# Optimization experiments

Hardware: AMD Instinct MI355X
Metric: run time of the kernel (lower is better)

## Reference

```python
import jax, jax.numpy as jnp
import numpy as np
import math

DIM = 1536
HEAD_DIM = 128
N_HEADS = DIM // HEAD_DIM
B, S = 2, 2048
F, H, W = 8, 16, 16  # F*H*W == S
MAX_POS = 1024
EPS = 1e-6


def _make_freqs():
    # complex rotary freqs per Wan convention, split [22,21,21] over head_dim/2=64
    c = HEAD_DIM // 2
    sizes = [c - 2 * (c // 3), c // 3, c // 3]
    theta = 10000.0
    parts = []
    for s in sizes:
        inv = 1.0 / theta ** (np.arange(s, dtype=np.float64) / s)
        ang = np.arange(MAX_POS, dtype=np.float64)[:, None] * inv[None, :]
        parts.append(np.stack([np.cos(ang), np.sin(ang)], axis=-1))
    return jnp.asarray(np.concatenate(parts, axis=1), dtype=jnp.float32)  # [MAX_POS, 64, 2]


def setup_inputs() -> dict:
    key = jax.random.key(0)
    ks = jax.random.split(key, 12)
    std = 1.0 / math.sqrt(DIM)
    inp = {
        "x": jax.random.normal(ks[0], (B, S, DIM), jnp.float32),
        "seq_lens": jnp.full((B,), S, jnp.int32),
        "grid_sizes": jnp.tile(jnp.array([[F, H, W]], jnp.int32), (B, 1)),
        "freqs": _make_freqs(),
        "Wq": jax.random.normal(ks[1], (DIM, DIM), jnp.float32) * std,
        "bq": jnp.zeros((DIM,), jnp.float32),
        "Wk": jax.random.normal(ks[2], (DIM, DIM), jnp.float32) * std,
        "bk": jnp.zeros((DIM,), jnp.float32),
        "Wv": jax.random.normal(ks[3], (DIM, DIM), jnp.float32) * std,
        "bv": jnp.zeros((DIM,), jnp.float32),
        "Wo": jax.random.normal(ks[4], (DIM, DIM), jnp.float32) * std,
        "bo": jnp.zeros((DIM,), jnp.float32),
        "wq_norm": jnp.ones((DIM,), jnp.float32),
        "wk_norm": jnp.ones((DIM,), jnp.float32),
    }
    return inp


def _rmsnorm(x, w):
    x32 = x.astype(jnp.float32)
    return x32 * jax.lax.rsqrt(jnp.mean(x32 * x32, axis=-1, keepdims=True) + EPS) * w


def _rope_apply(x, grid_sizes, freqs):
    # x: [B, S, N, D]; grid sizes uniform across batch -> vectorized (no per-sample loop)
    f, h, w = (int(v) for v in np.asarray(grid_sizes)[0])
    s_rot = f * h * w
    Bx, Sx, N, D = x.shape
    c = D // 2
    s0, s1 = c - 2 * (c // 3), c // 3
    cos, sin = freqs[..., 0], freqs[..., 1]

    def grid_cs(t):  # build [s_rot, c] table
        tf = jnp.broadcast_to(t[:f, None, None, :s0], (f, h, w, s0))
        th = jnp.broadcast_to(t[None, :h, None, s0:s0 + s1], (f, h, w, s1))
        tw = jnp.broadcast_to(t[None, None, :w, s0 + s1:s0 + 2 * s1], (f, h, w, s1))
        return jnp.concatenate([tf, th, tw], axis=-1).reshape(s_rot, 1, c)

    fc, fs = grid_cs(cos), grid_cs(sin)  # [s_rot, 1, c]
    xr = x[:, :s_rot].astype(jnp.float32).reshape(Bx, s_rot, N, c, 2)
    a, b = xr[..., 0], xr[..., 1]
    out = jnp.stack([a * fc - b * fs, a * fs + b * fc], axis=-1).reshape(Bx, s_rot, N, D)
    if s_rot < Sx:
        out = jnp.concatenate([out, x[:, s_rot:].astype(jnp.float32)], axis=1)
    return out


def reference(x, seq_lens, grid_sizes, freqs, Wq, bq, Wk, bk, Wv, bv, Wo, bo, wq_norm, wk_norm):
    Bx, Sx, dim = x.shape
    N, D = N_HEADS, HEAD_DIM
    q = _rmsnorm(x @ Wq.T + bq, wq_norm).reshape(Bx, Sx, N, D)
    k = _rmsnorm(x @ Wk.T + bk, wk_norm).reshape(Bx, Sx, N, D)
    v = (x @ Wv.T + bv).reshape(Bx, Sx, N, D)
    q = _rope_apply(q, grid_sizes, freqs)
    k = _rope_apply(k, grid_sizes, freqs)
    scores = jnp.einsum("bsnd,btnd->bnst", q, k) / math.sqrt(D)  # [B,N,S,S]
    kmask = jnp.arange(Sx)[None, :] < seq_lens[:, None]          # [B,S] over keys
    scores = jnp.where(kmask[:, None, None, :], scores, -1e30)
    attn = jax.nn.softmax(scores, axis=-1)
    out = jnp.einsum("bnst,btnd->bsnd", attn, v).reshape(Bx, Sx, dim)
    return out @ Wo.T + bo
```

## Files before the change

kernel.cpp:

```cpp
#include <hip/hip_runtime.h>

typedef __attribute__((ext_vector_type(8))) short bf16x8;
typedef __attribute__((ext_vector_type(8))) unsigned short ushort8;
typedef __attribute__((ext_vector_type(4))) float f32x4;
typedef __attribute__((ext_vector_type(16))) float f32x16;
typedef unsigned short u16;
typedef unsigned int u32;

__device__ inline float bf2f(u16 u) {
    unsigned int x = ((unsigned int)u) << 16;
    float f; __builtin_memcpy(&f, &x, 4); return f;
}
__device__ inline u16 f2bf(float f) {
    unsigned int x; __builtin_memcpy(&x, &f, 4);
    unsigned int r = (x + 0x7FFFu + ((x >> 16) & 1u)) >> 16;
    return (u16)r;
}
__device__ inline u32 cvtpk(float lo, float hi) {
    u32 r;
    asm("v_cvt_pk_bf16_f32 %0, %1, %2" : "=v"(r) : "v"(lo), "v"(hi));
    return r;
}
__device__ inline void store_out(u16* p, float v) { *p = f2bf(v); }
__device__ inline void store_out(float* p, float v) { *p = v; }

__global__ __launch_bounds__(256) void f32_to_bf16_kernel(const float* __restrict__ src,
                                                          u16* __restrict__ dst, int n8) {
    int i = blockIdx.x * 256 + threadIdx.x;
    if (i >= n8) return;
    float4 a = *(const float4*)(src + (size_t)i * 8);
    float4 b = *(const float4*)(src + (size_t)i * 8 + 4);
    ushort8 o;
    o[0] = f2bf(a.x); o[1] = f2bf(a.y); o[2] = f2bf(a.z); o[3] = f2bf(a.w);
    o[4] = f2bf(b.x); o[5] = f2bf(b.y); o[6] = f2bf(b.z); o[7] = f2bf(b.w);
    *(ushort8*)(dst + (size_t)i * 8) = o;
}

__global__ __launch_bounds__(256) void build_rope_kernel(const float* __restrict__ freqs,
                                                         float* __restrict__ rope) {
    int i = blockIdx.x * 256 + threadIdx.x;
    int s = i >> 6, j = i & 63;
    int fi = s >> 8, hi = (s >> 4) & 15, wi = s & 15;
    int pos = (j < 22) ? fi : ((j < 43) ? hi : wi);
    rope[s * 128 + j * 2]     = freqs[pos * 128 + j * 2];
    rope[s * 128 + j * 2 + 1] = freqs[pos * 128 + j * 2 + 1];
}

template <typename OutT>
__global__ __launch_bounds__(256) void gemm_bt(const u16* __restrict__ A, const u16* __restrict__ Bw,
                                               const float* __restrict__ bias, OutT* __restrict__ C,
                                               int M, int N, int K) {
    __shared__ __align__(16) u16 As[128 * 32];
    __shared__ __align__(16) u16 Bs[128 * 32];
    const int tid = threadIdx.x;
    const int w = tid >> 6, l = tid & 63;
    const int lg = l >> 4, li = l & 15;
    const int row0 = blockIdx.x * 128, col0 = blockIdx.y * 128;
    const int wr = (w >> 1) * 64, wc = (w & 1) * 64;

    f32x4 acc[4][4] = {};

    for (int k0 = 0; k0 < K; k0 += 32) {
#pragma unroll
        for (int c = 0; c < 2; ++c) {
            int idx = c * 256 + tid;
            int r = idx >> 2, col8 = (idx & 3) * 8;
            const u16* ga = A + (size_t)(row0 + r) * K + k0 + col8;
            const u16* gb = Bw + (size_t)(col0 + r) * K + k0 + col8;
            __builtin_amdgcn_global_load_lds((const __attribute__((address_space(1))) void*)ga,
                (__attribute__((address_space(3))) void*)((char*)As + c * 4096 + w * 1024), 16, 0, 0);
            __builtin_amdgcn_global_load_lds((const __attribute__((address_space(1))) void*)gb,
                (__attribute__((address_space(3))) void*)((char*)Bs + c * 4096 + w * 1024), 16, 0, 0);
        }
        __syncthreads();
        bf16x8 af[4], bfr[4];
#pragma unroll
        for (int m = 0; m < 4; ++m) af[m] = *(const bf16x8*)(As + (wr + m * 16 + li) * 32 + lg * 8);
#pragma unroll
        for (int n = 0; n < 4; ++n) bfr[n] = *(const bf16x8*)(Bs + (wc + n * 16 + li) * 32 + lg * 8);
#pragma unroll
        for (int m = 0; m < 4; ++m)
#pragma unroll
            for (int n = 0; n < 4; ++n)
                acc[m][n] = __builtin_amdgcn_mfma_f32_16x16x32_bf16(af[m], bfr[n], acc[m][n], 0, 0, 0);
        __syncthreads();
    }

#pragma unroll
    for (int m = 0; m < 4; ++m) {
#pragma unroll
        for (int n = 0; n < 4; ++n) {
#pragma unroll
            for (int j = 0; j < 4; ++j) {
                int r = row0 + wr + m * 16 + lg * 4 + j;
                int cc = col0 + wc + n * 16 + li;
                float v = acc[m][n][j] + bias[cc];
                store_out(&C[(size_t)r * N + cc], v);
            }
        }
    }
}

__global__ __launch_bounds__(256) void rmsrope_kernel(const u16* __restrict__ qkv,
                                                      const float* __restrict__ wq_n,
                                                      const float* __restrict__ wk_n,
                                                      const float* __restrict__ rope,
                                                      u16* __restrict__ qh, u16* __restrict__ kh) {
    int row = blockIdx.x;
    int b = row >> 11, s = row & 2047;
    int t = threadIdx.x;
    const u16* pr = qkv + (size_t)row * 4608;
    int c0 = t * 6;

    float q[6], k[6];
#pragma unroll
    for (int i = 0; i < 3; ++i) {
        ushort2 uq = *(const ushort2*)(pr + c0 + 2 * i);
        ushort2 uk = *(const ushort2*)(pr + 1536 + c0 + 2 * i);
        q[2 * i] = bf2f(uq.x); q[2 * i + 1] = bf2f(uq.y);
        k[2 * i] = bf2f(uk.x); k[2 * i + 1] = bf2f(uk.y);
    }
    float sq = 0.f, sk = 0.f;
#pragma unroll
    for (int i = 0; i < 6; ++i) { sq += q[i] * q[i]; sk += k[i] * k[i]; }
#pragma unroll
    for (int off = 32; off >= 1; off >>= 1) {
        sq += __shfl_down(sq, off);
        sk += __shfl_down(sk, off);
    }
    __shared__ float red[8];
    int w = t >> 6, l = t & 63;
    if (l == 0) { red[w] = sq; red[w + 4] = sk; }
    __syncthreads();
    float rq = rsqrtf((red[0] + red[1] + red[2] + red[3]) * (1.0f / 1536.0f) + 1e-6f);
    float rk = rsqrtf((red[4] + red[5] + red[6] + red[7]) * (1.0f / 1536.0f) + 1e-6f);

#pragma unroll
    for (int i = 0; i < 3; ++i) {
        int c = c0 + 2 * i;
        int h = c >> 7, d = c & 127;
        float cs = rope[s * 128 + d];
        float sn = rope[s * 128 + d + 1];
        float qa = q[2 * i] * rq * wq_n[c], qb = q[2 * i + 1] * rq * wq_n[c + 1];
        float ka = k[2 * i] * rk * wk_n[c], kb = k[2 * i + 1] * rk * wk_n[c + 1];
        size_t o = ((size_t)(b * 12 + h) * 2048 + s) * 128 + d;
        ushort2 qo, ko;
        qo.x = f2bf(qa * cs - qb * sn); qo.y = f2bf(qa * sn + qb * cs);
        ko.x = f2bf(ka * cs - kb * sn); ko.y = f2bf(ka * sn + kb * cs);
        *(ushort2*)(qh + o) = qo;
        *(ushort2*)(kh + o) = ko;
    }
}

__global__ __launch_bounds__(256) void vtrans_kernel(const u16* __restrict__ qkv,
                                                     u16* __restrict__ vt) {
    const int s0 = blockIdx.x * 64;
    const int d0 = blockIdx.y * 64;
    const int bh = blockIdx.z;
    const int b = bh / 12, h = bh % 12;
    const int t = threadIdx.x;

    __shared__ __align__(16) u16 L[64 * 72];

#pragma unroll
    for (int j = 0; j < 2; ++j) {
        int idx = j * 256 + t;
        int s = idx >> 3, c8 = idx & 7;
        ushort8 v8 = *(const ushort8*)(qkv + (size_t)(b * 2048 + s0 + s) * 4608 + 3072 + h * 128 + d0 + c8 * 8);
        int pb = c8 ^ ((s >> 3) & 7);
        *(ushort8*)(L + s * 72 + pb * 8) = v8;
    }
    __syncthreads();
#pragma unroll
    for (int j = 0; j < 2; ++j) {
        int idx = j * 256 + t;
        int d = idx >> 3, s8 = idx & 7;
        ushort8 o;
#pragma unroll
        for (int i = 0; i < 8; ++i) {
            int ps = s8 * 8 + i;
            int v4 = ps & 15;
            int ls = (ps & ~15) | (v4 & 3) | ((v4 & 4) << 1) | ((v4 & 8) >> 1);
            o[i] = L[ls * 72 + ((((d >> 3) ^ (ls >> 3)) & 7) << 3) + (d & 7)];
        }
        *(ushort8*)(vt + (size_t)bh * 128 * 2048 + (size_t)(d0 + d) * 2048 + s0 + s8 * 8) = o;
    }
}

__global__ __launch_bounds__(128, 2) void attn_kernel(const u16* __restrict__ qh, const u16* __restrict__ kh,
                                                      const u16* __restrict__ vt, const int* __restrict__ seq_lens,
                                                      u16* __restrict__ aout) {
    const int qt = blockIdx.x;
    const int bh = blockIdx.y;
    const int b = bh / 12, h = bh % 12;
    const int tid = threadIdx.x;
    const int w = tid >> 6, l = tid & 63;
    const int q5 = l & 31;
    const int hi = l >> 5;
    const int seqlen = seq_lens[b];

    __shared__ __align__(16) char smem[32768];
    u16* Ks = (u16*)smem;
    u16* Vs = (u16*)(smem + 16384);

    const size_t hbase = (size_t)bh * 2048 * 128;
    const u16* kb = kh + hbase;
    const u16* vtb = vt + hbase;

    const int qrow = qt * 64 + w * 32 + q5;
    bf16x8 qf[8];
    {
        const u16* qp = qh + hbase + (size_t)qrow * 128 + hi * 8;
#pragma unroll
        for (int kd = 0; kd < 8; ++kd) qf[kd] = *(const bf16x8*)(qp + kd * 16);
    }

    f32x16 oacc[4] = {};
    float m_run = -3e38f, l_run = 0.f;
    const float c2 = 0.08838834764831845f * 1.44269504088896341f;

    for (int kv0 = 0; kv0 < 2048; kv0 += 64) {
        __syncthreads();
#pragma unroll
        for (int i = 0; i < 8; ++i) {
            int p = i * 128 + tid;
            int kr = p >> 4, kc = p & 15;
            __builtin_amdgcn_global_load_lds(
                (const __attribute__((address_space(1))) void*)(kb + (size_t)(kv0 + kr) * 128 + ((kc ^ (kr & 15)) << 3)),
                (__attribute__((address_space(3))) void*)((char*)Ks + (i * 128 + w * 64) * 16), 16, 0, 0);
            int vr = p >> 3, vc = p & 7;
            __builtin_amdgcn_global_load_lds(
                (const __attribute__((address_space(1))) void*)(vtb + (size_t)vr * 2048 + kv0 + ((vc ^ (vr & 7)) << 3)),
                (__attribute__((address_space(3))) void*)((char*)Vs + (i * 128 + w * 64) * 16), 16, 0, 0);
        }
        __syncthreads();

        f32x16 sacc[2] = {};
#pragma unroll
        for (int t = 0; t < 2; ++t) {
            int row = t * 32 + q5;
#pragma unroll
            for (int kd = 0; kd < 8; ++kd) {
                int bk = (2 * kd + hi) ^ (q5 & 15);
                bf16x8 kf = *(const bf16x8*)(Ks + row * 128 + bk * 8);
                sacc[t] = __builtin_amdgcn_mfma_f32_32x32x16_bf16(kf, qf[kd], sacc[t], 0, 0, 0);
            }
        }

        if (kv0 + 64 > seqlen) {
#pragma unroll
            for (int t = 0; t < 2; ++t)
#pragma unroll
                for (int m = 0; m < 4; ++m)
#pragma unroll
                    for (int r = 0; r < 4; ++r) {
                        int kv = kv0 + t * 32 + m * 8 + hi * 4 + r;
                        if (kv >= seqlen) sacc[t][m * 4 + r] = -1e30f;
                    }
        }

        float pmax = sacc[0][0];
#pragma unroll
        for (int t = 0; t < 2; ++t)
#pragma unroll
            for (int r = 0; r < 16; ++r) pmax = fmaxf(pmax, sacc[t][r]);
        pmax = fmaxf(pmax, __shfl_xor(pmax, 32));

        int defer = __all(pmax <= m_run + 62.7f);
        if (!defer) {
            float mnew = fmaxf(m_run, pmax);
            float alpha = __builtin_amdgcn_exp2f((m_run - mnew) * c2);
#pragma unroll
            for (int dt = 0; dt < 4; ++dt)
#pragma unroll
                for (int r = 0; r < 16; ++r) oacc[dt][r] *= alpha;
            l_run *= alpha;
            m_run = mnew;
        }

        float ls = 0.f;
        u32 Wp[2][4][2];
#pragma unroll
        for (int t = 0; t < 2; ++t)
#pragma unroll
            for (int m = 0; m < 4; ++m) {
                float p0 = __builtin_amdgcn_exp2f((sacc[t][4 * m + 0] - m_run) * c2);
                float p1 = __builtin_amdgcn_exp2f((sacc[t][4 * m + 1] - m_run) * c2);
                float p2 = __builtin_amdgcn_exp2f((sacc[t][4 * m + 2] - m_run) * c2);
                float p3 = __builtin_amdgcn_exp2f((sacc[t][4 * m + 3] - m_run) * c2);
                ls += (p0 + p1) + (p2 + p3);
                Wp[t][m][0] = cvtpk(p0, p1);
                Wp[t][m][1] = cvtpk(p2, p3);
            }
        ls += __shfl_xor(ls, 32);
        l_run += ls;

#pragma unroll
        for (int t = 0; t < 2; ++t)
#pragma unroll
            for (int c = 0; c < 2; ++c) {
                union { u32 u[4]; bf16x8 v; } pu;
                pu.u[0] = Wp[t][2 * c][0]; pu.u[1] = Wp[t][2 * c][1];
                pu.u[2] = Wp[t][2 * c + 1][0]; pu.u[3] = Wp[t][2 * c + 1][1];
                int bk = 4 * t + 2 * c + hi;
#pragma unroll
                for (int dt = 0; dt < 4; ++dt) {
                    int drow = dt * 32 + q5;
                    int pb = bk ^ (drow & 7);
                    bf16x8 vf = *(const bf16x8*)(Vs + drow * 64 + pb * 8);
                    oacc[dt] = __builtin_amdgcn_mfma_f32_32x32x16_bf16(vf, pu.v, oacc[dt], 0, 0, 0);
                }
            }
    }

    __syncthreads();
    u32* Lq = (u32*)smem + w * 2144;
    float inv_l = 1.0f / l_run;
#pragma unroll
    for (int dt = 0; dt < 4; ++dt)
#pragma unroll
        for (int m = 0; m < 4; ++m) {
            u32 w0 = cvtpk(oacc[dt][4 * m + 0] * inv_l, oacc[dt][4 * m + 1] * inv_l);
            u32 w1 = cvtpk(oacc[dt][4 * m + 2] * inv_l, oacc[dt][4 * m + 3] * inv_l);
            int widx = dt * 16 + 4 * m + 2 * hi;
            Lq[q5 * 67 + widx] = w0;
            Lq[q5 * 67 + widx + 1] = w1;
        }
    __builtin_amdgcn_s_waitcnt(0);
#pragma unroll
    for (int pp = 0; pp < 8; ++pp) {
        int qq = pp * 4 + (l >> 4);
        int cc = l & 15;
        union { u32 u[4]; ushort8 v; } ou;
        ou.u[0] = Lq[qq * 67 + cc * 4 + 0];
        ou.u[1] = Lq[qq * 67 + cc * 4 + 1];
        ou.u[2] = Lq[qq * 67 + cc * 4 + 2];
        ou.u[3] = Lq[qq * 67 + cc * 4 + 3];
        size_t off = ((size_t)(b * 2048 + qt * 64 + w * 32 + qq)) * 1536 + h * 128 + cc * 8;
        *(ushort8*)(aout + off) = ou.v;
    }
}

extern "C" void kernel_launch(void* const* d_in, const int* in_sizes, int n_in,
                              void* d_out, int out_size, void* d_ws, size_t ws_size,
                              hipStream_t stream) {
    const float* x    = (const float*)d_in[0];
    const int* seqlen = (const int*)d_in[1];
    const float* freqs = (const float*)d_in[3];
    const float* Wq = (const float*)d_in[4];  const float* bq = (const float*)d_in[5];
    const float* Wk = (const float*)d_in[6];  const float* bk = (const float*)d_in[7];
    const float* Wv = (const float*)d_in[8];  const float* bv = (const float*)d_in[9];
    const float* Wo = (const float*)d_in[10]; const float* bo = (const float*)d_in[11];
    const float* wqn = (const float*)d_in[12];
    const float* wkn = (const float*)d_in[13];
    float* out = (float*)d_out;

    char* ws = (char*)d_ws;
    u16*   xb   = (u16*)(ws);
    u16*   wqkv = (u16*)(ws + 12582912);
    u16*   wob  = (u16*)(ws + 26738688);
    float* bqkv = (float*)(ws + 31457280);
    float* rope = (float*)(ws + 31475712);
    u16*   qkv  = (u16*)(ws + 32524288);
    u16*   qhb  = (u16*)(ws + 70273024);
    u16*   khb  = (u16*)(ws + 82855936);
    u16*   vtb  = (u16*)(ws + 95438848);
    u16*   aob  = (u16*)(ws + 108021760);

    f32_to_bf16_kernel<<<3072, 256, 0, stream>>>(x, xb, 786432);
    f32_to_bf16_kernel<<<1152, 256, 0, stream>>>(Wq, wqkv, 294912);
    f32_to_bf16_kernel<<<1152, 256, 0, stream>>>(Wk, wqkv + 2359296, 294912);
    f32_to_bf16_kernel<<<1152, 256, 0, stream>>>(Wv, wqkv + 4718592, 294912);
    f32_to_bf16_kernel<<<1152, 256, 0, stream>>>(Wo, wob, 294912);
    hipMemcpyAsync(bqkv,        bq, 1536 * 4, hipMemcpyDeviceToDevice, stream);
    hipMemcpyAsync(bqkv + 1536, bk, 1536 * 4, hipMemcpyDeviceToDevice, stream);
    hipMemcpyAsync(bqkv + 3072, bv, 1536 * 4, hipMemcpyDeviceToDevice, stream);
    build_rope_kernel<<<512, 256, 0, stream>>>(freqs, rope);

    gemm_bt<u16><<<dim3(32, 36), 256, 0, stream>>>(xb, wqkv, bqkv, qkv, 4096, 4608, 1536);
    rmsrope_kernel<<<4096, 256, 0, stream>>>(qkv, wqn, wkn, rope, qhb, khb);
    vtrans_kernel<<<dim3(32, 2, 24), 256, 0, stream>>>(qkv, vtb);
    attn_kernel<<<dim3(32, 24), 128, 0, stream>>>(qhb, khb, vtb, seqlen, aob);
    gemm_bt<float><<<dim3(32, 12), 256, 0, stream>>>(aob, wob, bo, out, 4096, 1536, 1536);
}
```

Measured before the change: 249.4 us.

## Pipeline GEMM and attention LDS loads, widen attention blocks, fuse weight conversions

The GEMM now uses a triple-buffered LDS ring, issuing global-to-LDS loads two tiles ahead with vmcnt waits and raw barriers instead of full syncthreads. The attention kernel moves to 4 waves per block covering 128 queries, with double-buffered K/V tiles and setprio around the MFMA sections, so memory latency overlaps compute and each K/V tile is shared by more queries. The four weight-conversion launches are merged into one kernel. In exchange, LDS use grows (48KB GEMM, 64KB attention), which may cap occupancy, and there are half as many attention blocks (384).

```diff
diff --git a/kernel.cpp b/kernel.cpp
--- a/kernel.cpp
+++ b/kernel.cpp
@@ -36,6 +36,21 @@
     *(ushort8*)(dst + (size_t)i * 8) = o;
 }
 
+__global__ __launch_bounds__(256) void wconv_kernel(const float* __restrict__ Wq, const float* __restrict__ Wk,
+                                                    const float* __restrict__ Wv, const float* __restrict__ Wo,
+                                                    u16* __restrict__ wqkv, u16* __restrict__ wob) {
+    int i = blockIdx.x * 256 + threadIdx.x;
+    int seg = i / 294912, j = i - seg * 294912;
+    const float* src = (seg == 0) ? Wq : (seg == 1) ? Wk : (seg == 2) ? Wv : Wo;
+    u16* dst = (seg < 3) ? (wqkv + (size_t)seg * 2359296) : wob;
+    float4 a = *(const float4*)(src + (size_t)j * 8);
+    float4 b = *(const float4*)(src + (size_t)j * 8 + 4);
+    ushort8 o;
+    o[0] = f2bf(a.x); o[1] = f2bf(a.y); o[2] = f2bf(a.z); o[3] = f2bf(a.w);
+    o[4] = f2bf(b.x); o[5] = f2bf(b.y); o[6] = f2bf(b.z); o[7] = f2bf(b.w);
+    *(ushort8*)(dst + (size_t)j * 8) = o;
+}
+
 __global__ __launch_bounds__(256) void build_rope_kernel(const float* __restrict__ freqs,
                                                          float* __restrict__ rope) {
     int i = blockIdx.x * 256 + threadIdx.x;
@@ -50,40 +65,63 @@
 __global__ __launch_bounds__(256) void gemm_bt(const u16* __restrict__ A, const u16* __restrict__ Bw,
                                                const float* __restrict__ bias, OutT* __restrict__ C,
                                                int M, int N, int K) {
-    __shared__ __align__(16) u16 As[128 * 32];
-    __shared__ __align__(16) u16 Bs[128 * 32];
+    __shared__ __align__(16) u16 As[3][4096];
+    __shared__ __align__(16) u16 Bs[3][4096];
     const int tid = threadIdx.x;
     const int w = tid >> 6, l = tid & 63;
     const int lg = l >> 4, li = l & 15;
     const int row0 = blockIdx.x * 128, col0 = blockIdx.y * 128;
     const int wr = (w >> 1) * 64, wc = (w & 1) * 64;
+    const int nt = K >> 5;
 
     f32x4 acc[4][4] = {};
 
-    for (int k0 = 0; k0 < K; k0 += 32) {
+    auto STAGE = [&](int bi, int t) {
+        int k0 = t << 5;
 #pragma unroll
         for (int c = 0; c < 2; ++c) {
             int idx = c * 256 + tid;
             int r = idx >> 2, col8 = (idx & 3) * 8;
-            const u16* ga = A + (size_t)(row0 + r) * K + k0 + col8;
-            const u16* gb = Bw + (size_t)(col0 + r) * K + k0 + col8;
-            __builtin_amdgcn_global_load_lds((const __attribute__((address_space(1))) void*)ga,
-                (__attribute__((address_space(3))) void*)((char*)As + c * 4096 + w * 1024), 16, 0, 0);
-            __builtin_amdgcn_global_load_lds((const __attribute__((address_space(1))) void*)gb,
-                (__attribute__((address_space(3))) void*)((char*)Bs + c * 4096 + w * 1024), 16, 0, 0);
-        }
-        __syncthreads();
-        bf16x8 af[4], bfr[4];
-#pragma unroll
-        for (int m = 0; m < 4; ++m) af[m] = *(const bf16x8*)(As + (wr + m * 16 + li) * 32 + lg * 8);
-#pragma unroll
-        for (int n = 0; n < 4; ++n) bfr[n] = *(const bf16x8*)(Bs + (wc + n * 16 + li) * 32 + lg * 8);
-#pragma unroll
-        for (int m = 0; m < 4; ++m)
-#pragma unroll
-            for (int n = 0; n < 4; ++n)
-                acc[m][n] = __builtin_amdgcn_mfma_f32_16x16x32_bf16(af[m], bfr[n], acc[m][n], 0, 0, 0);
-        __syncthreads();
+            __builtin_amdgcn_global_load_lds(
+                (const __attribute__((address_space(1))) void*)(A + (size_t)(row0 + r) * K + k0 + col8),
+                (__attribute__((address_space(3))) void*)((char*)&As[0][0] + bi * 8192 + c * 4096 + w * 1024), 16, 0, 0);
+            __builtin_amdgcn_global_load_lds(
+                (const __attribute__((address_space(1))) void*)(Bw + (size_t)(col0 + r) * K + k0 + col8),
+                (__attribute__((address_space(3))) void*)((char*)&Bs[0][0] + bi * 8192 + c * 4096 + w * 1024), 16, 0, 0);
+        }
+    };
+
+    STAGE(0, 0);
+    STAGE(1, 1);
+    for (int tb = 0; tb < nt; tb += 3) {
+#pragma unroll
+        for (int j = 0; j < 3; ++j) {
+            const int t = tb + j;
+            if (t + 2 < nt) {
+                STAGE((j + 2) % 3, t + 2);
+                asm volatile("s_waitcnt vmcnt(8)" ::: "memory");
+            } else if (t + 1 < nt) {
+                asm volatile("s_waitcnt vmcnt(4)" ::: "memory");
+            } else {
+                asm volatile("s_waitcnt vmcnt(0)" ::: "memory");
+            }
+            __builtin_amdgcn_s_barrier();
+            __builtin_amdgcn_sched_barrier(0);
+            const u16* as = &As[j][0];
+            const u16* bs = &Bs[j][0];
+            bf16x8 af[4], bfr[4];
+#pragma unroll
+            for (int m = 0; m < 4; ++m) af[m] = *(const bf16x8*)(as + (wr + m * 16 + li) * 32 + lg * 8);
+#pragma unroll
+            for (int n = 0; n < 4; ++n) bfr[n] = *(const bf16x8*)(bs + (wc + n * 16 + li) * 32 + lg * 8);
+#pragma unroll
+            for (int m = 0; m < 4; ++m)
+#pragma unroll
+                for (int n = 0; n < 4; ++n)
+                    acc[m][n] = __builtin_amdgcn_mfma_f32_16x16x32_bf16(af[m], bfr[n], acc[m][n], 0, 0, 0);
+            __builtin_amdgcn_sched_barrier(0);
+            __builtin_amdgcn_s_barrier();
+        }
     }
 
 #pragma unroll
@@ -187,7 +225,7 @@
     }
 }
 
-__global__ __launch_bounds__(128, 2) void attn_kernel(const u16* __restrict__ qh, const u16* __restrict__ kh,
+__global__ __launch_bounds__(256, 2) void attn_kernel(const u16* __restrict__ qh, const u16* __restrict__ kh,
                                                       const u16* __restrict__ vt, const int* __restrict__ seq_lens,
                                                       u16* __restrict__ aout) {
     const int qt = blockIdx.x;
@@ -199,15 +237,13 @@
     const int hi = l >> 5;
     const int seqlen = seq_lens[b];
 
-    __shared__ __align__(16) char smem[32768];
-    u16* Ks = (u16*)smem;
-    u16* Vs = (u16*)(smem + 16384);
+    __shared__ __align__(16) char smem[65536];
 
     const size_t hbase = (size_t)bh * 2048 * 128;
     const u16* kb = kh + hbase;
     const u16* vtb = vt + hbase;
 
-    const int qrow = qt * 64 + w * 32 + q5;
+    const int qrow = qt * 128 + w * 32 + q5;
     bf16x8 qf[8];
     {
         const u16* qp = qh + hbase + (size_t)qrow * 128 + hi * 8;
@@ -215,55 +251,72 @@
         for (int kd = 0; kd < 8; ++kd) qf[kd] = *(const bf16x8*)(qp + kd * 16);
     }
 
+    auto STAGE = [&](int bi, int kv0) {
+#pragma unroll
+        for (int i = 0; i < 4; ++i) {
+            int p = i * 256 + tid;
+            int kr = p >> 4, kc = p & 15;
+            __builtin_amdgcn_global_load_lds(
+                (const __attribute__((address_space(1))) void*)(kb + (size_t)(kv0 + kr) * 128 + ((kc ^ (kr & 15)) << 3)),
+                (__attribute__((address_space(3))) void*)(smem + bi * 16384 + i * 4096 + w * 1024), 16, 0, 0);
+            int vr = p >> 3, vc = p & 7;
+            __builtin_amdgcn_global_load_lds(
+                (const __attribute__((address_space(1))) void*)(vtb + (size_t)vr * 2048 + kv0 + ((vc ^ (vr & 7)) << 3)),
+                (__attribute__((address_space(3))) void*)(smem + 32768 + bi * 16384 + i * 4096 + w * 1024), 16, 0, 0);
+        }
+    };
+
     f32x16 oacc[4] = {};
     float m_run = -3e38f, l_run = 0.f;
     const float c2 = 0.08838834764831845f * 1.44269504088896341f;
 
-    for (int kv0 = 0; kv0 < 2048; kv0 += 64) {
-        __syncthreads();
-#pragma unroll
-        for (int i = 0; i < 8; ++i) {
-            int p = i * 128 + tid;
-            int kr = p >> 4, kc = p & 15;
-            __builtin_amdgcn_global_load_lds(
-                (const __attribute__((address_space(1))) void*)(kb + (size_t)(kv0 + kr) * 128 + ((kc ^ (kr & 15)) << 3)),
-                (__attribute__((address_space(3))) void*)((char*)Ks + (i * 128 + w * 64) * 16), 16, 0, 0);
-            int vr = p >> 3, vc = p & 7;
-            __builtin_amdgcn_global_load_lds(
-                (const __attribute__((address_space(1))) void*)(vtb + (size_t)vr * 2048 + kv0 + ((vc ^ (vr & 7)) << 3)),
-                (__attribute__((address_space(3))) void*)((char*)Vs + (i * 128 + w * 64) * 16), 16, 0, 0);
-        }
-        __syncthreads();
+    STAGE(0, 0);
+    for (int t = 0; t < 32; ++t) {
+        const int cur = t & 1;
+        const int kv0 = t * 64;
+        if (t < 31) {
+            STAGE(cur ^ 1, kv0 + 64);
+            asm volatile("s_waitcnt vmcnt(8)" ::: "memory");
+        } else {
+            asm volatile("s_waitcnt vmcnt(0)" ::: "memory");
+        }
+        __builtin_amdgcn_s_barrier();
+        __builtin_amdgcn_sched_barrier(0);
+
+        const u16* Ks = (const u16*)(smem + cur * 16384);
+        const u16* Vs = (const u16*)(smem + 32768 + cur * 16384);
 
         f32x16 sacc[2] = {};
-#pragma unroll
-        for (int t = 0; t < 2; ++t) {
-            int row = t * 32 + q5;
+        __builtin_amdgcn_s_setprio(1);
+#pragma unroll
+        for (int tt = 0; tt < 2; ++tt) {
+            int row = tt * 32 + q5;
 #pragma unroll
             for (int kd = 0; kd < 8; ++kd) {
                 int bk = (2 * kd + hi) ^ (q5 & 15);
                 bf16x8 kf = *(const bf16x8*)(Ks + row * 128 + bk * 8);
-                sacc[t] = __builtin_amdgcn_mfma_f32_32x32x16_bf16(kf, qf[kd], sacc[t], 0, 0, 0);
+                sacc[tt] = __builtin_amdgcn_mfma_f32_32x32x16_bf16(kf, qf[kd], sacc[tt], 0, 0, 0);
             }
         }
+        __builtin_amdgcn_s_setprio(0);
 
         if (kv0 + 64 > seqlen) {
 #pragma unroll
-            for (int t = 0; t < 2; ++t)
+            for (int tt = 0; tt < 2; ++tt)
 #pragma unroll
                 for (int m = 0; m < 4; ++m)
 #pragma unroll
                     for (int r = 0; r < 4; ++r) {
-                        int kv = kv0 + t * 32 + m * 8 + hi * 4 + r;
-                        if (kv >= seqlen) sacc[t][m * 4 + r] = -1e30f;
+                        int kv = kv0 + tt * 32 + m * 8 + hi * 4 + r;
+                        if (kv >= seqlen) sacc[tt][m * 4 + r] = -1e30f;
                     }
         }
 
         float pmax = sacc[0][0];
 #pragma unroll
-        for (int t = 0; t < 2; ++t)
-#pragma unroll
-            for (int r = 0; r < 16; ++r) pmax = fmaxf(pmax, sacc[t][r]);
+        for (int tt = 0; tt < 2; ++tt)
+#pragma unroll
+            for (int r = 0; r < 16; ++r) pmax = fmaxf(pmax, sacc[tt][r]);
         pmax = fmaxf(pmax, __shfl_xor(pmax, 32));
 
         int defer = __all(pmax <= m_run + 62.7f);
@@ -281,28 +334,29 @@
         float ls = 0.f;
         u32 Wp[2][4][2];
 #pragma unroll
-        for (int t = 0; t < 2; ++t)
+        for (int tt = 0; tt < 2; ++tt)
 #pragma unroll
             for (int m = 0; m < 4; ++m) {
-                float p0 = __builtin_amdgcn_exp2f((sacc[t][4 * m + 0] - m_run) * c2);
-                float p1 = __builtin_amdgcn_exp2f((sacc[t][4 * m + 1] - m_run) * c2);
-                float p2 = __builtin_amdgcn_exp2f((sacc[t][4 * m + 2] - m_run) * c2);
-                float p3 = __builtin_amdgcn_exp2f((sacc[t][4 * m + 3] - m_run) * c2);
+                float p0 = __builtin_amdgcn_exp2f((sacc[tt][4 * m + 0] - m_run) * c2);
+                float p1 = __builtin_amdgcn_exp2f((sacc[tt][4 * m + 1] - m_run) * c2);
+                float p2 = __builtin_amdgcn_exp2f((sacc[tt][4 * m + 2] - m_run) * c2);
+                float p3 = __builtin_amdgcn_exp2f((sacc[tt][4 * m + 3] - m_run) * c2);
                 ls += (p0 + p1) + (p2 + p3);
-                Wp[t][m][0] = cvtpk(p0, p1);
-                Wp[t][m][1] = cvtpk(p2, p3);
+                Wp[tt][m][0] = cvtpk(p0, p1);
+                Wp[tt][m][1] = cvtpk(p2, p3);
             }
         ls += __shfl_xor(ls, 32);
         l_run += ls;
 
-#pragma unroll
-        for (int t = 0; t < 2; ++t)
+        __builtin_amdgcn_s_setprio(1);
+#pragma unroll
+        for (int tt = 0; tt < 2; ++tt)
 #pragma unroll
             for (int c = 0; c < 2; ++c) {
                 union { u32 u[4]; bf16x8 v; } pu;
-                pu.u[0] = Wp[t][2 * c][0]; pu.u[1] = Wp[t][2 * c][1];
-                pu.u[2] = Wp[t][2 * c + 1][0]; pu.u[3] = Wp[t][2 * c + 1][1];
-                int bk = 4 * t + 2 * c + hi;
+                pu.u[0] = Wp[tt][2 * c][0]; pu.u[1] = Wp[tt][2 * c][1];
+                pu.u[2] = Wp[tt][2 * c + 1][0]; pu.u[3] = Wp[tt][2 * c + 1][1];
+                int bk = 4 * tt + 2 * c + hi;
 #pragma unroll
                 for (int dt = 0; dt < 4; ++dt) {
                     int drow = dt * 32 + q5;
@@ -311,6 +365,9 @@
                     oacc[dt] = __builtin_amdgcn_mfma_f32_32x32x16_bf16(vf, pu.v, oacc[dt], 0, 0, 0);
                 }
             }
+        __builtin_amdgcn_s_setprio(0);
+        __builtin_amdgcn_sched_barrier(0);
+        __builtin_amdgcn_s_barrier();
     }
 
     __syncthreads();
@@ -336,7 +393,7 @@
         ou.u[1] = Lq[qq * 67 + cc * 4 + 1];
         ou.u[2] = Lq[qq * 67 + cc * 4 + 2];
         ou.u[3] = Lq[qq * 67 + cc * 4 + 3];
-        size_t off = ((size_t)(b * 2048 + qt * 64 + w * 32 + qq)) * 1536 + h * 128 + cc * 8;
+        size_t off = ((size_t)(b * 2048 + qt * 128 + w * 32 + qq)) * 1536 + h * 128 + cc * 8;
         *(ushort8*)(aout + off) = ou.v;
     }
 }
@@ -368,10 +425,7 @@
     u16*   aob  = (u16*)(ws + 108021760);
 
     f32_to_bf16_kernel<<<3072, 256, 0, stream>>>(x, xb, 786432);
-    f32_to_bf16_kernel<<<1152, 256, 0, stream>>>(Wq, wqkv, 294912);
-    f32_to_bf16_kernel<<<1152, 256, 0, stream>>>(Wk, wqkv + 2359296, 294912);
-    f32_to_bf16_kernel<<<1152, 256, 0, stream>>>(Wv, wqkv + 4718592, 294912);
-    f32_to_bf16_kernel<<<1152, 256, 0, stream>>>(Wo, wob, 294912);
+    wconv_kernel<<<4608, 256, 0, stream>>>(Wq, Wk, Wv, Wo, wqkv, wob);
     hipMemcpyAsync(bqkv,        bq, 1536 * 4, hipMemcpyDeviceToDevice, stream);
     hipMemcpyAsync(bqkv + 1536, bk, 1536 * 4, hipMemcpyDeviceToDevice, stream);
     hipMemcpyAsync(bqkv + 3072, bv, 1536 * 4, hipMemcpyDeviceToDevice, stream);
@@ -380,6 +434,6 @@
     gemm_bt<u16><<<dim3(32, 36), 256, 0, stream>>>(xb, wqkv, bqkv, qkv, 4096, 4608, 1536);
     rmsrope_kernel<<<4096, 256, 0, stream>>>(qkv, wqn, wkn, rope, qhb, khb);
     vtrans_kernel<<<dim3(32, 2, 24), 256, 0, stream>>>(qkv, vtb);
-    attn_kernel<<<dim3(32, 24), 128, 0, stream>>>(qhb, khb, vtb, seqlen, aob);
+    attn_kernel<<<dim3(16, 24), 256, 0, stream>>>(qhb, khb, vtb, seqlen, aob);
     gemm_bt<float><<<dim3(32, 12), 256, 0, stream>>>(aob, wob, bo, out, 4096, 1536, 1536);
 }
```

Result: faster. 228.5 us (-8.4%).
